# Performance work log

Hardware: AMD Instinct MI355X
Metric: run time of the kernel (lower is better)

Reference implementation:

```python
import jax, jax.numpy as jnp
import numpy as np

N_NODES = 100000
N_EDGES = 1600000
IN_FEATS = 256
HEADS = 4
OUT_FEATS = 32
NEG_SLOPE = 0.2


def setup_inputs() -> dict:
    key = jax.random.key(0)
    k = jax.random.split(key, 7)
    feat = jax.random.normal(k[0], (N_NODES, IN_FEATS), dtype=jnp.float32)
    src = jax.random.randint(k[1], (N_EDGES,), 0, N_NODES)
    dst = jax.random.randint(k[2], (N_EDGES,), 0, N_NODES)
    W = jax.random.normal(k[3], (HEADS * OUT_FEATS, IN_FEATS), dtype=jnp.float32) * 0.05
    attn_l = jax.random.normal(k[4], (1, HEADS, OUT_FEATS), dtype=jnp.float32) * 0.1
    attn_r = jax.random.normal(k[5], (1, HEADS, OUT_FEATS), dtype=jnp.float32) * 0.1
    bias = jnp.zeros((HEADS * OUT_FEATS,), dtype=jnp.float32)
    return {"feat": feat, "src": src, "dst": dst, "W": W,
            "attn_l": attn_l, "attn_r": attn_r, "bias": bias}


def reference(feat, src, dst, W, attn_l, attn_r, bias):
    N = feat.shape[0]
    H, F = attn_l.shape[1], attn_l.shape[2]
    # linear projection: [N, H*F] -> [N, H, F]
    ft = (feat @ W.T).reshape(N, H, F)
    # per-node attention scores [N, H]
    el = jnp.sum(ft * attn_l, axis=-1)
    er = jnp.sum(ft * attn_r, axis=-1)
    # edge scores: u_add_v + LeakyReLU, [E, H]
    e = el[src] + er[dst]
    e = jnp.where(e >= 0, e, NEG_SLOPE * e)
    # edge softmax segmented by destination node
    emax = jax.ops.segment_max(e, dst, num_segments=N)  # [N, H]
    emax = jnp.where(jnp.isfinite(emax), emax, 0.0)
    ex = jnp.exp(e - emax[dst])  # [E, H]
    esum = jax.ops.segment_sum(ex, dst, num_segments=N)  # [N, H]
    a = ex / jnp.maximum(esum[dst], 1e-16)  # [E, H]
    # weighted scatter-sum aggregation: u_mul_e + sum
    msg = ft[src] * a[:, :, None]  # [E, H, F]
    rst = jax.ops.segment_sum(msg, dst, num_segments=N)  # [N, H, F]
    rst = rst + bias.reshape(1, H, F)
    return rst


if __name__ == "__main__":
    out = reference(**setup_inputs())
    print(out.shape, out.dtype)
```

## Files before the change

### kernel.cpp

```cpp
#include <hip/hip_runtime.h>

#define NEG_SLOPE 0.2f
#define G_SHIFT 8
#define G_SIZE  256
#define NB1     256

typedef __attribute__((ext_vector_type(8))) short short8;
typedef __attribute__((ext_vector_type(4))) float floatx4;

__device__ inline unsigned short f32_to_bf16(float f) {
    union { float f; unsigned int u; } c; c.f = f;
    unsigned int u = c.u;
    u += 0x7FFFu + ((u >> 16) & 1u);
    return (unsigned short)(u >> 16);
}
__device__ inline float bf16_lo(unsigned int u) {
    union { unsigned int u; float f; } c; c.u = u << 16; return c.f;
}
__device__ inline float bf16_hi(unsigned int u) {
    union { unsigned int u; float f; } c; c.u = u & 0xFFFF0000u; return c.f;
}

__global__ __launch_bounds__(256) void k_wconv(const float* __restrict__ W,
                                               unsigned short* __restrict__ Wb,
                                               int n) {
    int i = blockIdx.x * 256 + threadIdx.x;
    if (i < n) Wb[i] = f32_to_bf16(W[i]);
}

__global__ __launch_bounds__(256) void k_gemm_mfma(const float* __restrict__ feat,
                                                   const unsigned short* __restrict__ Wb,
                                                   unsigned short* __restrict__ ftb,
                                                   int M) {
    __shared__ float Abuf[8][2048];

    const int tid  = threadIdx.x;
    const int w    = tid >> 6;
    const int lane = tid & 63;
    const int l16  = lane & 15;
    const int quad = lane >> 4;
    const int wm   = w & 1;
    const int wn   = w >> 1;
    const int tile = blockIdx.x * 64;

    short8 b[4][8];
#pragma unroll
    for (int t = 0; t < 4; ++t) {
        const unsigned short* bp =
            Wb + (size_t)((wn * 4 + t) * 16 + l16) * 256 + quad * 8;
#pragma unroll
        for (int kc = 0; kc < 8; ++kc)
            b[t][kc] = *(const short8*)(bp + kc * 32);
    }

    const int rloc = lane >> 3;
    const int c4   = ((lane & 7) ^ rloc) * 4;
    int gr0 = tile + (w * 2 + 0) * 8 + rloc; if (gr0 >= M) gr0 = M - 1;
    int gr1 = tile + (w * 2 + 1) * 8 + rloc; if (gr1 >= M) gr1 = M - 1;
    const float* g0 = feat + (size_t)gr0 * 256 + c4;
    const float* g1 = feat + (size_t)gr1 * 256 + c4;

#define STAGE(JC) do {                                                          \
    __builtin_amdgcn_global_load_lds(                                           \
        (const __attribute__((address_space(1))) unsigned int*)(g0 + (JC) * 32),\
        (__attribute__((address_space(3))) unsigned int*)&Abuf[(JC)][(w * 2 + 0) * 256], \
        16, 0, 0);                                                              \
    __builtin_amdgcn_global_load_lds(                                           \
        (const __attribute__((address_space(1))) unsigned int*)(g1 + (JC) * 32),\
        (__attribute__((address_space(3))) unsigned int*)&Abuf[(JC)][(w * 2 + 1) * 256], \
        16, 0, 0);                                                              \
} while (0)

    floatx4 acc[2][4];
#pragma unroll
    for (int m = 0; m < 2; ++m)
#pragma unroll
        for (int t = 0; t < 4; ++t)
            acc[m][t] = (floatx4){0.f, 0.f, 0.f, 0.f};

    STAGE(0); STAGE(1); STAGE(2); STAGE(3);
    STAGE(4); STAGE(5); STAGE(6); STAGE(7);

    const int sw = (l16 & 7) << 4;

#define KSTEP(J, VM) do {                                                       \
    asm volatile("s_waitcnt vmcnt(" #VM ")" ::: "memory");                      \
    __builtin_amdgcn_s_barrier();                                               \
    asm volatile("" ::: "memory");                                              \
    const char* ab = (const char*)&Abuf[(J)][0];                                \
    _Pragma("unroll")                                                           \
    for (int m = 0; m < 2; ++m) {                                               \
        int base = (wm * 32 + m * 16 + l16) * 128 + quad * 32;                  \
        float4 alo = *(const float4*)(ab + ((base)      ^ sw));                 \
        float4 ahi = *(const float4*)(ab + ((base + 16) ^ sw));                 \
        short8 af;                                                              \
        af[0] = (short)f32_to_bf16(alo.x);                                      \
        af[1] = (short)f32_to_bf16(alo.y);                                      \
        af[2] = (short)f32_to_bf16(alo.z);                                      \
        af[3] = (short)f32_to_bf16(alo.w);                                      \
        af[4] = (short)f32_to_bf16(ahi.x);                                      \
        af[5] = (short)f32_to_bf16(ahi.y);                                      \
        af[6] = (short)f32_to_bf16(ahi.z);                                      \
        af[7] = (short)f32_to_bf16(ahi.w);                                      \
        _Pragma("unroll")                                                       \
        for (int t = 0; t < 4; ++t)                                             \
            acc[m][t] = __builtin_amdgcn_mfma_f32_16x16x32_bf16(                \
                af, b[t][(J)], acc[m][t], 0, 0, 0);                             \
    }                                                                           \
} while (0)

    KSTEP(0, 14); KSTEP(1, 12); KSTEP(2, 10); KSTEP(3, 8);
    KSTEP(4,  6); KSTEP(5,  4); KSTEP(6,  2); KSTEP(7, 0);

#undef KSTEP
#undef STAGE

#pragma unroll
    for (int m = 0; m < 2; ++m) {
#pragma unroll
        for (int t = 0; t < 4; ++t) {
#pragma unroll
            for (int r = 0; r < 4; ++r) {
                int row = tile + wm * 32 + m * 16 + quad * 4 + r;
                if (row < M)
                    ftb[(size_t)row * 128 + (wn * 4 + t) * 16 + l16] =
                        f32_to_bf16(acc[m][t][r]);
            }
        }
    }
}

__global__ __launch_bounds__(256) void k_elr(const unsigned short* __restrict__ ftb,
                                             const float* __restrict__ al,
                                             const float* __restrict__ ar,
                                             float* __restrict__ el,
                                             float* __restrict__ er,
                                             int NH) {
    int i = blockIdx.x * 256 + threadIdx.x;
    if (i >= NH) return;
    int h = i & 3;
    const unsigned int* f = (const unsigned int*)ftb + (size_t)i * 16;
    const float* lp = al + h * 32;
    const float* rp = ar + h * 32;
    float sl = 0.f, sr = 0.f;
#pragma unroll
    for (int j = 0; j < 16; ++j) {
        unsigned int u = f[j];
        float f0 = bf16_lo(u), f1 = bf16_hi(u);
        sl += f0 * lp[2 * j] + f1 * lp[2 * j + 1];
        sr += f0 * rp[2 * j] + f1 * rp[2 * j + 1];
    }
    el[i] = sl;
    er[i] = sr;
}

__global__ __launch_bounds__(256) void k_count(const int* __restrict__ dst,
                                               int* __restrict__ counts,
                                               int E, int CH, int B) {
    __shared__ int hist[512];
    int j = blockIdx.x, t = threadIdx.x;
    for (int bk = t; bk < B; bk += 256) hist[bk] = 0;
    __syncthreads();
    int lo = j * CH, hi = min(E, lo + CH);
    for (int i = lo + t; i < hi; i += 256)
        atomicAdd(&hist[dst[i] >> G_SHIFT], 1);
    __syncthreads();
    for (int bk = t; bk < B; bk += 256) counts[bk * NB1 + j] = hist[bk];
}

__global__ __launch_bounds__(256) void k_scan1(const int* __restrict__ deg,
                                               int* __restrict__ offs,
                                               int* __restrict__ bsum, int n) {
    __shared__ int ls[256];
    int b = blockIdx.x, t = threadIdx.x;
    int base = b * 1024 + t * 4;
    int d0 = (base + 0 < n) ? deg[base + 0] : 0;
    int d1 = (base + 1 < n) ? deg[base + 1] : 0;
    int d2 = (base + 2 < n) ? deg[base + 2] : 0;
    int d3 = (base + 3 < n) ? deg[base + 3] : 0;
    int s = d0 + d1 + d2 + d3;
    ls[t] = s;
    __syncthreads();
    for (int o = 1; o < 256; o <<= 1) {
        int v = (t >= o) ? ls[t - o] : 0;
        __syncthreads();
        ls[t] += v;
        __syncthreads();
    }
    int excl = ls[t] - s;
    if (base + 0 < n) offs[base + 0] = excl;
    if (base + 1 < n) offs[base + 1] = excl + d0;
    if (base + 2 < n) offs[base + 2] = excl + d0 + d1;
    if (base + 3 < n) offs[base + 3] = excl + d0 + d1 + d2;
    if (t == 255) bsum[b] = ls[255];
}

__global__ __launch_bounds__(256) void k_scan2(int* __restrict__ bsum, int NB) {
    __shared__ int ls[256];
    int t = threadIdx.x;
    int v = (t < NB) ? bsum[t] : 0;
    ls[t] = v;
    __syncthreads();
    for (int o = 1; o < 256; o <<= 1) {
        int u = (t >= o) ? ls[t - o] : 0;
        __syncthreads();
        ls[t] += u;
        __syncthreads();
    }
    if (t < NB) bsum[t] = ls[t] - v;
}

__global__ __launch_bounds__(256) void k_partition(const int* __restrict__ src,
                                                   const int* __restrict__ dst,
                                                   const int* __restrict__ scanned,
                                                   const int* __restrict__ bsum,
                                                   int* __restrict__ part,
                                                   int E, int CH, int B) {
    __shared__ int curs[512];
    int j = blockIdx.x, t = threadIdx.x;
    for (int bk = t; bk < B; bk += 256) {
        int idx = bk * NB1 + j;
        curs[bk] = scanned[idx] + bsum[idx >> 10];
    }
    __syncthreads();
    int lo = j * CH, hi = min(E, lo + CH);
    for (int i = lo + t; i < hi; i += 256) {
        int d = dst[i];
        int bk = d >> G_SHIFT;
        int pos = atomicAdd(&curs[bk], 1);
        if (pos >= 0 && pos < E)
            part[pos] = ((d & (G_SIZE - 1)) << 17) | src[i];
    }
}

__global__ __launch_bounds__(256) void k_bucket(const int* __restrict__ scanned,
                                                const int* __restrict__ bsum,
                                                const int* __restrict__ part,
                                                int* __restrict__ offs,
                                                int* __restrict__ esrc,
                                                int E, int B, int N) {
    __shared__ int hist[256], ls[256], curs[256];
    int b = blockIdx.x, t = threadIdx.x;
    int i0 = b * NB1;
    int start = scanned[i0] + bsum[i0 >> 10];
    int end = E;
    if (b < B - 1) {
        int i1 = (b + 1) * NB1;
        end = scanned[i1] + bsum[i1 >> 10];
    }

    hist[t] = 0;
    __syncthreads();
    for (int i = start + t; i < end; i += 256)
        atomicAdd(&hist[(part[i] >> 17) & 255], 1);
    __syncthreads();

    int h = hist[t];
    ls[t] = h;
    __syncthreads();
    for (int o = 1; o < 256; o <<= 1) {
        int v = (t >= o) ? ls[t - o] : 0;
        __syncthreads();
        ls[t] += v;
        __syncthreads();
    }
    int excl = ls[t] - h;
    curs[t] = excl;
    int node = b * G_SIZE + t;
    if (node < N) offs[node] = start + excl;
    if (b == B - 1 && t == 0) offs[N] = E;
    __syncthreads();

    for (int i = start + t; i < end; i += 256) {
        int p = part[i];
        int pos = start + atomicAdd(&curs[(p >> 17) & 255], 1);
        if (pos >= 0 && pos < E) esrc[pos] = p & 0x1FFFF;
    }
}

__global__ __launch_bounds__(256) void k_aggr_csr(const int* __restrict__ offs,
                                                  const int* __restrict__ esrc,
                                                  const float* __restrict__ el,
                                                  const float* __restrict__ er,
                                                  const unsigned short* __restrict__ ftb,
                                                  const float* __restrict__ bias,
                                                  float* __restrict__ out,
                                                  int N) {
    int node = blockIdx.x * 4 + (threadIdx.x >> 6);
    if (node >= N) return;
    int lane = threadIdx.x & 63;
    int h1 = lane & 3;
    int h2b = (lane >> 4) << 2;
    float er1 = er[node * 4 + h1];

    int start = offs[node];
    int deg   = offs[node + 1] - start;

    float2 acc = make_float2(0.f, 0.f);
    float  wsum = 0.f;
    const unsigned int* ftu = (const unsigned int*)ftb;

    int p = 0;
    while (p < deg) {
        int cnt = min(16, deg - p);
        float w = 0.f;
        int   s = 0;
        int   e = lane >> 2;
        if (e < cnt) {
            s = esrc[start + p + e];
            float x = el[s * 4 + h1] + er1;
            x = x >= 0.f ? x : NEG_SLOPE * x;
            w = __expf(x);
        }
        float        wv[16];
        unsigned int uv[16];
#pragma unroll
        for (int j = 0; j < 16; ++j) {
            int ib = (j << 4) + h2b;
            wv[j] = __int_as_float(
                __builtin_amdgcn_ds_bpermute(ib, __float_as_int(w)));
            int sj = __builtin_amdgcn_ds_bpermute(ib, s);
            uv[j] = ftu[(size_t)sj * 64 + lane];
        }
#pragma unroll
        for (int j = 0; j < 16; ++j) {
            wsum  += wv[j];
            acc.x += wv[j] * bf16_lo(uv[j]);
            acc.y += wv[j] * bf16_hi(uv[j]);
        }
        p += cnt;
    }
    float scale = 1.0f / fmaxf(wsum, 1e-16f);
    float2 bv = ((const float2*)bias)[lane];
    float2 o;
    o.x = acc.x * scale + bv.x;
    o.y = acc.y * scale + bv.y;
    ((float2*)out)[(size_t)node * 64 + lane] = o;
}

__global__ __launch_bounds__(256) void k_init_fb(float* __restrict__ out,
                                                 const float* __restrict__ bias,
                                                 float* __restrict__ esum,
                                                 int n_out, int n_esum) {
    int i = blockIdx.x * 256 + threadIdx.x;
    if (i < n_out)  out[i]  = bias[i & 127];
    if (i < n_esum) esum[i] = 0.0f;
}

__global__ __launch_bounds__(256) void k_esum_fb(const int* __restrict__ src,
                                                 const int* __restrict__ dst,
                                                 const float* __restrict__ el,
                                                 const float* __restrict__ er,
                                                 float* __restrict__ esum,
                                                 int E4) {
    int i = blockIdx.x * 256 + threadIdx.x;
    if (i >= E4) return;
    int e = i >> 2, h = i & 3;
    int s = src[e], d = dst[e];
    float x = el[s * 4 + h] + er[d * 4 + h];
    x = x >= 0.f ? x : NEG_SLOPE * x;
    atomicAdd(&esum[d * 4 + h], __expf(x));
}

__global__ __launch_bounds__(256) void k_aggr_fb(const int* __restrict__ src,
                                                 const int* __restrict__ dst,
                                                 const float* __restrict__ el,
                                                 const float* __restrict__ er,
                                                 const float* __restrict__ esum,
                                                 const unsigned short* __restrict__ ftb,
                                                 float* __restrict__ out,
                                                 int E) {
    int i = blockIdx.x * 256 + threadIdx.x;
    int e = i >> 6;
    if (e >= E) return;
    int c = i & 63;
    int h = c >> 4;
    int s = src[e], d = dst[e];
    float x = el[s * 4 + h] + er[d * 4 + h];
    x = x >= 0.f ? x : NEG_SLOPE * x;
    float a = __expf(x) / fmaxf(esum[d * 4 + h], 1e-16f);
    unsigned int u = ((const unsigned int*)ftb)[(size_t)s * 64 + c];
    float* o = out + (size_t)d * 128 + c * 2;
    atomicAdd(o + 0, bf16_lo(u) * a);
    atomicAdd(o + 1, bf16_hi(u) * a);
}

extern "C" void kernel_launch(void* const* d_in, const int* in_sizes, int n_in,
                              void* d_out, int out_size, void* d_ws, size_t ws_size,
                              hipStream_t stream) {
    const float* feat   = (const float*)d_in[0];
    const int*   src    = (const int*)d_in[1];
    const int*   dst    = (const int*)d_in[2];
    const float* W      = (const float*)d_in[3];
    const float* attn_l = (const float*)d_in[4];
    const float* attn_r = (const float*)d_in[5];
    const float* bias   = (const float*)d_in[6];

    const int N  = in_sizes[0] / 256;
    const int E  = in_sizes[1];
    const int NW = in_sizes[3];
    float* out = (float*)d_out;

    const int B  = (N + G_SIZE - 1) / G_SIZE;
    const int CH = (E + NB1 - 1) / NB1;
    const int n2 = B * NB1;

    unsigned short* ftb = (unsigned short*)d_ws;
    unsigned short* Wb  = ftb + (size_t)N * 128;
    float* el = (float*)(Wb + NW);
    float* er = el + (size_t)N * 4;
    int* offs    = (int*)(er + (size_t)N * 4);
    int* counts  = offs + (N + 1);
    int* scanned = counts + n2;
    int* bsum    = scanned + n2;
    int* part    = bsum + 256;
    int* esrc    = part + E;
    size_t need = (size_t)((char*)(esrc + E) - (char*)d_ws);

    k_wconv<<<(NW + 255) / 256, 256, 0, stream>>>(W, Wb, NW);
    k_gemm_mfma<<<(N + 63) / 64, 256, 0, stream>>>(feat, Wb, ftb, N);
    k_elr<<<(N * 4 + 255) / 256, 256, 0, stream>>>(ftb, attn_l, attn_r, el, er, N * 4);

    if (ws_size >= need) {
        const int NBs = (n2 + 1023) / 1024;
        k_count<<<NB1, 256, 0, stream>>>(dst, counts, E, CH, B);
        k_scan1<<<NBs, 256, 0, stream>>>(counts, scanned, bsum, n2);
        k_scan2<<<1, 256, 0, stream>>>(bsum, NBs);
        k_partition<<<NB1, 256, 0, stream>>>(src, dst, scanned, bsum, part, E, CH, B);
        k_bucket<<<B, 256, 0, stream>>>(scanned, bsum, part, offs, esrc, E, B, N);
        k_aggr_csr<<<(N + 3) / 4, 256, 0, stream>>>(offs, esrc, el, er, ftb, bias, out, N);
    } else {
        float* esum = (float*)(er + (size_t)N * 4);
        k_init_fb<<<(N * 128 + 255) / 256, 256, 0, stream>>>(out, bias, esum, N * 128, N * 4);
        k_esum_fb<<<(E * 4 + 255) / 256, 256, 0, stream>>>(src, dst, el, er, esum, E * 4);
        k_aggr_fb<<<((size_t)E * 64 + 255) / 256, 256, 0, stream>>>(src, dst, el, er, esum, ftb, out, E);
    }
}
```

Baseline: 345.4 us.

## Fuse W conversion and attention scores into GEMM, merge sort stages via grid barrier

Converts W to bf16 inside the GEMM kernel and computes el/er from the fp32 accumulators with lane shuffles, which removes the separate conversion and score kernels and avoids re-reading the projected features. The five counting-sort kernels are merged into one persistent kernel of B blocks separated by software grid barriers, with the chunk count changed from 256 to B so each bucket block also does one chunk. This cuts launch overhead and intermediate traffic. The software barrier assumes all B (~391) blocks are co-resident, and it has a spin timeout that could silently break correctness if they are not.

```diff
diff --git a/kernel.cpp b/kernel.cpp
--- a/kernel.cpp
+++ b/kernel.cpp
@@ -3,7 +3,6 @@
 #define NEG_SLOPE 0.2f
 #define G_SHIFT 8
 #define G_SIZE  256
-#define NB1     256
 
 typedef __attribute__((ext_vector_type(8))) short short8;
 typedef __attribute__((ext_vector_type(4))) float floatx4;
@@ -21,17 +20,36 @@
     union { unsigned int u; float f; } c; c.u = u & 0xFFFF0000u; return c.f;
 }
 
-__global__ __launch_bounds__(256) void k_wconv(const float* __restrict__ W,
-                                               unsigned short* __restrict__ Wb,
-                                               int n) {
-    int i = blockIdx.x * 256 + threadIdx.x;
-    if (i < n) Wb[i] = f32_to_bf16(W[i]);
-}
-
-__global__ __launch_bounds__(256) void k_gemm_mfma(const float* __restrict__ feat,
-                                                   const unsigned short* __restrict__ Wb,
-                                                   unsigned short* __restrict__ ftb,
-                                                   int M) {
+__device__ inline void grid_sync(int* bar, int nb) {
+    __syncthreads();
+    if (threadIdx.x == 0) {
+        __threadfence();
+        int g = __hip_atomic_load(&bar[1], __ATOMIC_ACQUIRE, __HIP_MEMORY_SCOPE_AGENT);
+        int a = __hip_atomic_fetch_add(&bar[0], 1, __ATOMIC_ACQ_REL, __HIP_MEMORY_SCOPE_AGENT);
+        if (a == nb - 1) {
+            __hip_atomic_store(&bar[0], 0, __ATOMIC_RELAXED, __HIP_MEMORY_SCOPE_AGENT);
+            __hip_atomic_store(&bar[1], g + 1, __ATOMIC_RELEASE, __HIP_MEMORY_SCOPE_AGENT);
+        } else {
+            int spins = 0;
+            while (__hip_atomic_load(&bar[1], __ATOMIC_ACQUIRE, __HIP_MEMORY_SCOPE_AGENT) == g) {
+                __builtin_amdgcn_s_sleep(8);
+                if (++spins > (1 << 22)) break;
+            }
+        }
+        __threadfence();
+    }
+    __syncthreads();
+}
+
+__global__ __launch_bounds__(256) void k_gemm_fused(const float* __restrict__ feat,
+                                                    const float* __restrict__ W,
+                                                    const float* __restrict__ al,
+                                                    const float* __restrict__ ar,
+                                                    unsigned short* __restrict__ ftb,
+                                                    float* __restrict__ el,
+                                                    float* __restrict__ er,
+                                                    int* bar,
+                                                    int M) {
     __shared__ float Abuf[8][2048];
 
     const int tid  = threadIdx.x;
@@ -43,14 +61,27 @@
     const int wn   = w >> 1;
     const int tile = blockIdx.x * 64;
 
+    if (bar && blockIdx.x == 0 && tid == 0) { bar[0] = 0; bar[1] = 0; }
+
     short8 b[4][8];
 #pragma unroll
     for (int t = 0; t < 4; ++t) {
-        const unsigned short* bp =
-            Wb + (size_t)((wn * 4 + t) * 16 + l16) * 256 + quad * 8;
-#pragma unroll
-        for (int kc = 0; kc < 8; ++kc)
-            b[t][kc] = *(const short8*)(bp + kc * 32);
+        const float* bp = W + (size_t)((wn * 4 + t) * 16 + l16) * 256 + quad * 8;
+#pragma unroll
+        for (int kc = 0; kc < 8; ++kc) {
+            float4 w0 = *(const float4*)(bp + kc * 32);
+            float4 w1 = *(const float4*)(bp + kc * 32 + 4);
+            short8 bf;
+            bf[0] = (short)f32_to_bf16(w0.x);
+            bf[1] = (short)f32_to_bf16(w0.y);
+            bf[2] = (short)f32_to_bf16(w0.z);
+            bf[3] = (short)f32_to_bf16(w0.w);
+            bf[4] = (short)f32_to_bf16(w1.x);
+            bf[5] = (short)f32_to_bf16(w1.y);
+            bf[6] = (short)f32_to_bf16(w1.z);
+            bf[7] = (short)f32_to_bf16(w1.w);
+            b[t][kc] = bf;
+        }
     }
 
     const int rloc = lane >> 3;
@@ -128,153 +159,161 @@
             }
         }
     }
-}
-
-__global__ __launch_bounds__(256) void k_elr(const unsigned short* __restrict__ ftb,
-                                             const float* __restrict__ al,
-                                             const float* __restrict__ ar,
-                                             float* __restrict__ el,
-                                             float* __restrict__ er,
-                                             int NH) {
-    int i = blockIdx.x * 256 + threadIdx.x;
-    if (i >= NH) return;
-    int h = i & 3;
-    const unsigned int* f = (const unsigned int*)ftb + (size_t)i * 16;
-    const float* lp = al + h * 32;
-    const float* rp = ar + h * 32;
-    float sl = 0.f, sr = 0.f;
-#pragma unroll
-    for (int j = 0; j < 16; ++j) {
-        unsigned int u = f[j];
-        float f0 = bf16_lo(u), f1 = bf16_hi(u);
-        sl += f0 * lp[2 * j] + f1 * lp[2 * j + 1];
-        sr += f0 * rp[2 * j] + f1 * rp[2 * j + 1];
-    }
-    el[i] = sl;
-    er[i] = sr;
-}
-
-__global__ __launch_bounds__(256) void k_count(const int* __restrict__ dst,
-                                               int* __restrict__ counts,
-                                               int E, int CH, int B) {
-    __shared__ int hist[512];
-    int j = blockIdx.x, t = threadIdx.x;
-    for (int bk = t; bk < B; bk += 256) hist[bk] = 0;
+
+    const int h0 = wn * 2, h1 = wn * 2 + 1;
+    float al00 = al[h0 * 32 + l16],      al01 = al[h0 * 32 + 16 + l16];
+    float al10 = al[h1 * 32 + l16],      al11 = al[h1 * 32 + 16 + l16];
+    float ar00 = ar[h0 * 32 + l16],      ar01 = ar[h0 * 32 + 16 + l16];
+    float ar10 = ar[h1 * 32 + l16],      ar11 = ar[h1 * 32 + 16 + l16];
+#pragma unroll
+    for (int m = 0; m < 2; ++m) {
+#pragma unroll
+        for (int r = 0; r < 4; ++r) {
+            float p0 = acc[m][0][r] * al00 + acc[m][1][r] * al01;
+            float p1 = acc[m][2][r] * al10 + acc[m][3][r] * al11;
+            float q0 = acc[m][0][r] * ar00 + acc[m][1][r] * ar01;
+            float q1 = acc[m][2][r] * ar10 + acc[m][3][r] * ar11;
+#pragma unroll
+            for (int d = 1; d < 16; d <<= 1) {
+                p0 += __shfl_xor(p0, d, 16);
+                p1 += __shfl_xor(p1, d, 16);
+                q0 += __shfl_xor(q0, d, 16);
+                q1 += __shfl_xor(q1, d, 16);
+            }
+            if (l16 == 0) {
+                int row = tile + wm * 32 + m * 16 + quad * 4 + r;
+                if (row < M) {
+                    el[row * 4 + h0] = p0;
+                    el[row * 4 + h1] = p1;
+                    er[row * 4 + h0] = q0;
+                    er[row * 4 + h1] = q1;
+                }
+            }
+        }
+    }
+}
+
+__global__ __launch_bounds__(256, 2) void k_sort(const int* __restrict__ src,
+                                                 const int* __restrict__ dst,
+                                                 int* __restrict__ counts,
+                                                 int* __restrict__ scanned,
+                                                 int* __restrict__ bsum,
+                                                 int* __restrict__ part,
+                                                 int* __restrict__ offs,
+                                                 int* __restrict__ esrc,
+                                                 int* bar,
+                                                 int E, int B, int CH, int NBs,
+                                                 int N, int n2) {
+    __shared__ int smA[512];
+    __shared__ int smB[256];
+    const int j = blockIdx.x, t = threadIdx.x;
+
+    for (int bk = t; bk < B; bk += 256) smA[bk] = 0;
     __syncthreads();
-    int lo = j * CH, hi = min(E, lo + CH);
-    for (int i = lo + t; i < hi; i += 256)
-        atomicAdd(&hist[dst[i] >> G_SHIFT], 1);
+    {
+        int lo = j * CH, hi = min(E, lo + CH);
+        for (int i = lo + t; i < hi; i += 256)
+            atomicAdd(&smA[dst[i] >> G_SHIFT], 1);
+    }
     __syncthreads();
-    for (int bk = t; bk < B; bk += 256) counts[bk * NB1 + j] = hist[bk];
-}
-
-__global__ __launch_bounds__(256) void k_scan1(const int* __restrict__ deg,
-                                               int* __restrict__ offs,
-                                               int* __restrict__ bsum, int n) {
-    __shared__ int ls[256];
-    int b = blockIdx.x, t = threadIdx.x;
-    int base = b * 1024 + t * 4;
-    int d0 = (base + 0 < n) ? deg[base + 0] : 0;
-    int d1 = (base + 1 < n) ? deg[base + 1] : 0;
-    int d2 = (base + 2 < n) ? deg[base + 2] : 0;
-    int d3 = (base + 3 < n) ? deg[base + 3] : 0;
-    int s = d0 + d1 + d2 + d3;
-    ls[t] = s;
+    for (int bk = t; bk < B; bk += 256) counts[bk * B + j] = smA[bk];
+
+    grid_sync(bar, B);
+
+    if (j < NBs) {
+        int base = j * 1024 + t * 4;
+        int d0 = (base + 0 < n2) ? counts[base + 0] : 0;
+        int d1 = (base + 1 < n2) ? counts[base + 1] : 0;
+        int d2 = (base + 2 < n2) ? counts[base + 2] : 0;
+        int d3 = (base + 3 < n2) ? counts[base + 3] : 0;
+        int s = d0 + d1 + d2 + d3;
+        smA[t] = s;
+        __syncthreads();
+        for (int o = 1; o < 256; o <<= 1) {
+            int v = (t >= o) ? smA[t - o] : 0;
+            __syncthreads();
+            smA[t] += v;
+            __syncthreads();
+        }
+        int excl = smA[t] - s;
+        if (base + 0 < n2) scanned[base + 0] = excl;
+        if (base + 1 < n2) scanned[base + 1] = excl + d0;
+        if (base + 2 < n2) scanned[base + 2] = excl + d0 + d1;
+        if (base + 3 < n2) scanned[base + 3] = excl + d0 + d1 + d2;
+        if (t == 255) bsum[j] = smA[255];
+    }
+
+    grid_sync(bar, B);
+
+    if (j == 0) {
+        int v = (t < NBs) ? bsum[t] : 0;
+        smA[t] = v;
+        __syncthreads();
+        for (int o = 1; o < 256; o <<= 1) {
+            int u = (t >= o) ? smA[t - o] : 0;
+            __syncthreads();
+            smA[t] += u;
+            __syncthreads();
+        }
+        if (t < NBs) bsum[t] = smA[t] - v;
+    }
+
+    grid_sync(bar, B);
+
+    for (int bk = t; bk < B; bk += 256) {
+        int idx = bk * B + j;
+        smA[bk] = scanned[idx] + bsum[idx >> 10];
+    }
     __syncthreads();
-    for (int o = 1; o < 256; o <<= 1) {
-        int v = (t >= o) ? ls[t - o] : 0;
-        __syncthreads();
-        ls[t] += v;
-        __syncthreads();
-    }
-    int excl = ls[t] - s;
-    if (base + 0 < n) offs[base + 0] = excl;
-    if (base + 1 < n) offs[base + 1] = excl + d0;
-    if (base + 2 < n) offs[base + 2] = excl + d0 + d1;
-    if (base + 3 < n) offs[base + 3] = excl + d0 + d1 + d2;
-    if (t == 255) bsum[b] = ls[255];
-}
-
-__global__ __launch_bounds__(256) void k_scan2(int* __restrict__ bsum, int NB) {
-    __shared__ int ls[256];
-    int t = threadIdx.x;
-    int v = (t < NB) ? bsum[t] : 0;
-    ls[t] = v;
-    __syncthreads();
-    for (int o = 1; o < 256; o <<= 1) {
-        int u = (t >= o) ? ls[t - o] : 0;
-        __syncthreads();
-        ls[t] += u;
-        __syncthreads();
-    }
-    if (t < NB) bsum[t] = ls[t] - v;
-}
-
-__global__ __launch_bounds__(256) void k_partition(const int* __restrict__ src,
-                                                   const int* __restrict__ dst,
-                                                   const int* __restrict__ scanned,
-                                                   const int* __restrict__ bsum,
-                                                   int* __restrict__ part,
-                                                   int E, int CH, int B) {
-    __shared__ int curs[512];
-    int j = blockIdx.x, t = threadIdx.x;
-    for (int bk = t; bk < B; bk += 256) {
-        int idx = bk * NB1 + j;
-        curs[bk] = scanned[idx] + bsum[idx >> 10];
-    }
-    __syncthreads();
-    int lo = j * CH, hi = min(E, lo + CH);
-    for (int i = lo + t; i < hi; i += 256) {
-        int d = dst[i];
-        int bk = d >> G_SHIFT;
-        int pos = atomicAdd(&curs[bk], 1);
-        if (pos >= 0 && pos < E)
-            part[pos] = ((d & (G_SIZE - 1)) << 17) | src[i];
-    }
-}
-
-__global__ __launch_bounds__(256) void k_bucket(const int* __restrict__ scanned,
-                                                const int* __restrict__ bsum,
-                                                const int* __restrict__ part,
-                                                int* __restrict__ offs,
-                                                int* __restrict__ esrc,
-                                                int E, int B, int N) {
-    __shared__ int hist[256], ls[256], curs[256];
-    int b = blockIdx.x, t = threadIdx.x;
-    int i0 = b * NB1;
-    int start = scanned[i0] + bsum[i0 >> 10];
-    int end = E;
-    if (b < B - 1) {
-        int i1 = (b + 1) * NB1;
-        end = scanned[i1] + bsum[i1 >> 10];
-    }
-
-    hist[t] = 0;
-    __syncthreads();
-    for (int i = start + t; i < end; i += 256)
-        atomicAdd(&hist[(part[i] >> 17) & 255], 1);
-    __syncthreads();
-
-    int h = hist[t];
-    ls[t] = h;
-    __syncthreads();
-    for (int o = 1; o < 256; o <<= 1) {
-        int v = (t >= o) ? ls[t - o] : 0;
-        __syncthreads();
-        ls[t] += v;
-        __syncthreads();
-    }
-    int excl = ls[t] - h;
-    curs[t] = excl;
-    int node = b * G_SIZE + t;
-    if (node < N) offs[node] = start + excl;
-    if (b == B - 1 && t == 0) offs[N] = E;
-    __syncthreads();
-
-    for (int i = start + t; i < end; i += 256) {
-        int p = part[i];
-        int pos = start + atomicAdd(&curs[(p >> 17) & 255], 1);
-        if (pos >= 0 && pos < E) esrc[pos] = p & 0x1FFFF;
+    {
+        int lo = j * CH, hi = min(E, lo + CH);
+        for (int i = lo + t; i < hi; i += 256) {
+            int d = dst[i];
+            int bk = d >> G_SHIFT;
+            int pos = atomicAdd(&smA[bk], 1);
+            if (pos >= 0 && pos < E)
+                part[pos] = ((d & (G_SIZE - 1)) << 17) | src[i];
+        }
+    }
+
+    grid_sync(bar, B);
+
+    {
+        const int b = j;
+        int i0 = b * B;
+        int start = scanned[i0] + bsum[i0 >> 10];
+        int end = E;
+        if (b < B - 1) {
+            int i1 = (b + 1) * B;
+            end = scanned[i1] + bsum[i1 >> 10];
+        }
+
+        smA[t] = 0;
+        __syncthreads();
+        for (int i = start + t; i < end; i += 256)
+            atomicAdd(&smA[(part[i] >> 17) & 255], 1);
+        __syncthreads();
+
+        int h = smA[t];
+        __syncthreads();
+        for (int o = 1; o < 256; o <<= 1) {
+            int v = (t >= o) ? smA[t - o] : 0;
+            __syncthreads();
+            smA[t] += v;
+            __syncthreads();
+        }
+        int excl = smA[t] - h;
+        smB[t] = excl;
+        int node = b * G_SIZE + t;
+        if (node < N) offs[node] = start + excl;
+        if (b == B - 1 && t == 0) offs[N] = E;
+        __syncthreads();
+
+        for (int i = start + t; i < end; i += 256) {
+            int p = part[i];
+            int pos = start + atomicAdd(&smB[(p >> 17) & 255], 1);
+            if (pos >= 0 && pos < E) esrc[pos] = p & 0x1FFFF;
+        }
     }
 }
 
@@ -315,18 +354,18 @@
         float        wv[16];
         unsigned int uv[16];
 #pragma unroll
-        for (int j = 0; j < 16; ++j) {
-            int ib = (j << 4) + h2b;
-            wv[j] = __int_as_float(
+        for (int jj = 0; jj < 16; ++jj) {
+            int ib = (jj << 4) + h2b;
+            wv[jj] = __int_as_float(
                 __builtin_amdgcn_ds_bpermute(ib, __float_as_int(w)));
             int sj = __builtin_amdgcn_ds_bpermute(ib, s);
-            uv[j] = ftu[(size_t)sj * 64 + lane];
-        }
-#pragma unroll
-        for (int j = 0; j < 16; ++j) {
-            wsum  += wv[j];
-            acc.x += wv[j] * bf16_lo(uv[j]);
-            acc.y += wv[j] * bf16_hi(uv[j]);
+            uv[jj] = ftu[(size_t)sj * 64 + lane];
+        }
+#pragma unroll
+        for (int jj = 0; jj < 16; ++jj) {
+            wsum  += wv[jj];
+            acc.x += wv[jj] * bf16_lo(uv[jj]);
+            acc.y += wv[jj] * bf16_hi(uv[jj]);
         }
         p += cnt;
     }
@@ -398,37 +437,36 @@
 
     const int N  = in_sizes[0] / 256;
     const int E  = in_sizes[1];
-    const int NW = in_sizes[3];
     float* out = (float*)d_out;
 
-    const int B  = (N + G_SIZE - 1) / G_SIZE;
-    const int CH = (E + NB1 - 1) / NB1;
-    const int n2 = B * NB1;
+    const int B   = (N + G_SIZE - 1) / G_SIZE;
+    const int CH  = (E + B - 1) / B;
+    const int n2  = B * B;
+    const int NBs = (n2 + 1023) / 1024;
 
     unsigned short* ftb = (unsigned short*)d_ws;
-    unsigned short* Wb  = ftb + (size_t)N * 128;
-    float* el = (float*)(Wb + NW);
+    float* el = (float*)(ftb + (size_t)N * 128);
     float* er = el + (size_t)N * 4;
     int* offs    = (int*)(er + (size_t)N * 4);
     int* counts  = offs + (N + 1);
     int* scanned = counts + n2;
     int* bsum    = scanned + n2;
-    int* part    = bsum + 256;
+    int* bar     = bsum + 256;
+    int* part    = bar + 8;
     int* esrc    = part + E;
     size_t need = (size_t)((char*)(esrc + E) - (char*)d_ws);
 
-    k_wconv<<<(NW + 255) / 256, 256, 0, stream>>>(W, Wb, NW);
-    k_gemm_mfma<<<(N + 63) / 64, 256, 0, stream>>>(feat, Wb, ftb, N);
-    k_elr<<<(N * 4 + 255) / 256, 256, 0, stream>>>(ftb, attn_l, attn_r, el, er, N * 4);
-
-    if (ws_size >= need) {
-        const int NBs = (n2 + 1023) / 1024;
-        k_count<<<NB1, 256, 0, stream>>>(dst, counts, E, CH, B);
-        k_scan1<<<NBs, 256, 0, stream>>>(counts, scanned, bsum, n2);
-        k_scan2<<<1, 256, 0, stream>>>(bsum, NBs);
-        k_partition<<<NB1, 256, 0, stream>>>(src, dst, scanned, bsum, part, E, CH, B);
-        k_bucket<<<B, 256, 0, stream>>>(scanned, bsum, part, offs, esrc, E, B, N);
-        k_aggr_csr<<<(N + 3) / 4, 256, 0, stream>>>(offs, esrc, el, er, ftb, bias, out, N);
+    const int sorted = (ws_size >= need);
+
+    k_gemm_fused<<<(N + 63) / 64, 256, 0, stream>>>(feat, W, attn_l, attn_r,
+                                                    ftb, el, er,
+                                                    sorted ? bar : (int*)nullptr, N);
+
+    if (sorted) {
+        k_sort<<<B, 256, 0, stream>>>(src, dst, counts, scanned, bsum, part,
+                                      offs, esrc, bar, E, B, CH, NBs, N, n2);
+        k_aggr_csr<<<(N + 3) / 4, 256, 0, stream>>>(offs, esrc, el, er, ftb,
+                                                    bias, out, N);
     } else {
         float* esum = (float*)(er + (size_t)N * 4);
         k_init_fb<<<(N * 128 + 255) / 256, 256, 0, stream>>>(out, bias, esum, N * 128, N * 4);
```

Result: slower. 659.8 us (+91.0%).
